# Kernel tuning notes

Measured on AMD Instinct MI355X. Metric: run time of the kernel, lower is better.

The kernel has to match this reference:

```python
import jax, jax.numpy as jnp
import numpy as np

D = 1024
N_HEAD = 16
D_HEAD = D // N_HEAD
EPS = 1e-6


def setup_inputs() -> dict:
    key = jax.random.key(0)
    k1, k2, k3 = jax.random.split(key, 3)
    x = jax.random.normal(k1, (4, 1024, D), dtype=jnp.float32)
    # Linear weights stored as (in, out); y = x @ W
    Wqkv = jax.random.normal(k2, (D, 3 * D), dtype=jnp.float32) * (1.0 / np.sqrt(D))
    Wo = jax.random.normal(k3, (D, D), dtype=jnp.float32) * (1.0 / np.sqrt(D))
    scale_q = jnp.ones((D_HEAD,), dtype=jnp.float32)
    scale_k = jnp.ones((D_HEAD,), dtype=jnp.float32)
    return {"x": x, "Wqkv": Wqkv, "Wo": Wo, "scale_q": scale_q, "scale_k": scale_k}


def _rmsnorm_global(x, scale):
    # NOTE: faithful to source: mean over ALL elements (scalar RMS), not per-vector.
    rms = jnp.sqrt(jnp.mean(x * x))
    return (x / (rms + EPS)) * scale  # scale broadcasts over last dim (d_head)


def reference(x, Wqkv, Wo, scale_q, scale_k):
    b, s, d = x.shape
    qkv = x @ Wqkv  # (b, s, 3d)
    q, k, v = jnp.split(qkv, 3, axis=-1)
    q = q.reshape(b, s, N_HEAD, D_HEAD)
    k = k.reshape(b, s, N_HEAD, D_HEAD)
    v = v.reshape(b, s, N_HEAD, D_HEAD)
    q = _rmsnorm_global(q, scale_q)
    k = _rmsnorm_global(k, scale_k)
    # NOTE: no 1/sqrt(d_head) scaling, no mask (faithful to source)
    attn = jnp.einsum('bqhd,bkhd->bhqk', q, k)
    attn = jax.nn.softmax(attn, axis=-1)
    z = jnp.einsum('bhqk,bkhd->bqhd', attn, v)
    z = z.reshape(b, s, d)
    return z @ Wo
```

## Files before the change

kernel.cpp:

```cpp
#include <hip/hip_runtime.h>

typedef float f32x4 __attribute__((ext_vector_type(4)));
typedef short bf16x8 __attribute__((ext_vector_type(8)));
typedef _Float16 f16x8 __attribute__((ext_vector_type(8)));
typedef unsigned short u16;

__device__ __forceinline__ u16 f2bf(float f) {
  unsigned int u = __float_as_uint(f);
  u = u + 0x7fffu + ((u >> 16) & 1u);
  return (u16)(u >> 16);
}
__device__ __forceinline__ float bf2f(u16 h) {
  return __uint_as_float(((unsigned int)h) << 16);
}
__device__ __forceinline__ u16 f2h(float f) {
  _Float16 h = (_Float16)f;
  union { _Float16 h; u16 u; } cv;
  cv.h = h;
  return cv.u;
}

typedef unsigned int as1_uint __attribute__((address_space(1)));
typedef unsigned int as3_uint __attribute__((address_space(3)));
__device__ __forceinline__ void gl_lds16(const void* g, void* l) {
  __builtin_amdgcn_global_load_lds((as1_uint*)g, (as3_uint*)l, 16, 0, 0);
}


__global__ __launch_bounds__(256) void conv_x_kernel(const float* __restrict__ x,
                                                     u16* __restrict__ Xp) {
  const int g = blockIdx.x * 256 + threadIdx.x;
  const int o = g * 8;
  const int slab = o >> 17;
  const int rem = o & 131071;
  const int kstep = rem >> 12;
  const int rem2 = rem & 4095;
  const int r = rem2 >> 5;
  const int cp = (rem2 & 31) >> 3;
  const int c = cp ^ ((r >> 1) & 3);
  const int s = slab * 128 + r;
  const int k = kstep * 32 + c * 8;
  const float4 v0 = *(const float4*)&x[(size_t)s * 1024 + k];
  const float4 v1 = *(const float4*)&x[(size_t)s * 1024 + k + 4];
  ushort4 a, b;
  a.x = f2h(v0.x); a.y = f2h(v0.y); a.z = f2h(v0.z); a.w = f2h(v0.w);
  b.x = f2h(v1.x); b.y = f2h(v1.y); b.z = f2h(v1.z); b.w = f2h(v1.w);
  *(ushort4*)&Xp[o] = a;
  *(ushort4*)&Xp[o + 4] = b;
}

__global__ __launch_bounds__(256) void conv_w_kernel(
    const float* __restrict__ src, int ncols, u16* __restrict__ dst) {
  __shared__ float tl[64][132];
  const int t = threadIdx.x;
  const int slab = blockIdx.x, kg = blockIdx.y;
  const int n0 = slab * 128, k0 = kg * 64;
#pragma unroll
  for (int i = 0; i < 8; i++) {
    const int fidx = i * 256 + t;
    const int r = fidx >> 5, c4 = (fidx & 31) * 4;
    *(float4*)&tl[r][c4] = *(const float4*)&src[(size_t)(k0 + r) * ncols + n0 + c4];
  }
  __syncthreads();
  const size_t base = (size_t)slab * 131072 + (size_t)(kg * 2) * 4096;
#pragma unroll
  for (int i = 0; i < 4; i++) {
    const int g = i * 256 + t;
    const int img = g >> 9, ci = g & 511;
    const int r = ci >> 2, cp = ci & 3;
    const int c = cp ^ ((r >> 1) & 3);
    const int klc = img * 32 + c * 8;
    ushort4 h0, h1;
    float v[8];
#pragma unroll
    for (int e = 0; e < 8; e++) v[e] = tl[klc + e][r];
    h0.x = f2h(v[0]); h0.y = f2h(v[1]); h0.z = f2h(v[2]); h0.w = f2h(v[3]);
    h1.x = f2h(v[4]); h1.y = f2h(v[5]); h1.z = f2h(v[6]); h1.w = f2h(v[7]);
    *(ushort4*)&dst[base + g * 8] = h0;
    *(ushort4*)&dst[base + g * 8 + 4] = h1;
  }
}

__global__ __launch_bounds__(256) void gemm_qkv_kernel(
    const u16* __restrict__ Xp, const u16* __restrict__ Wp,
    u16* __restrict__ qf, u16* __restrict__ kf, u16* __restrict__ vT,
    const float* __restrict__ scale_q, const float* __restrict__ scale_k,
    float* __restrict__ sums) {
  __shared__ u16 Xs0[4096], Ws0[4096], Xs1[4096], Ws1[4096];
  const int tid = threadIdx.x, wv = tid >> 6, lane = tid & 63;
  const int lm = lane & 15, quad = lane >> 4;
  const int L = blockIdx.x;
  const int xcd = L & 7, idx = L >> 3;
  const int rr = idx & 7, cc8 = idx >> 3;
  const int bmS = (xcd & 3) * 8 + rr;
  const int bnS = (xcd >> 2) * 12 + cc8;
  const bool is_v = (bnS >= 16);
  const int wr = (wv >> 1) * 64, wc = (wv & 1) * 64;
  const int fq = (quad ^ ((lm >> 1) & 3)) * 8;
  const u16* Xg = Xp + (size_t)bmS * 131072;
  const u16* Wg = Wp + (size_t)bnS * 131072;
  const int dof0 = (wv * 2) * 512, dof1 = (wv * 2 + 1) * 512;
  const f32x4 z4 = {0.f, 0.f, 0.f, 0.f};
  f32x4 acc[4][4];
#pragma unroll
  for (int i = 0; i < 4; i++)
#pragma unroll
    for (int j = 0; j < 4; j++) acc[i][j] = z4;

#define ISSUE(t, Xs, Ws)                                   \
  do {                                                     \
    const size_t tb_ = (size_t)(t) * 4096;                 \
    gl_lds16(Xg + tb_ + dof0 + lane * 8, &Xs[dof0]);       \
    gl_lds16(Xg + tb_ + dof1 + lane * 8, &Xs[dof1]);       \
    gl_lds16(Wg + tb_ + dof0 + lane * 8, &Ws[dof0]);       \
    gl_lds16(Wg + tb_ + dof1 + lane * 8, &Ws[dof1]);       \
  } while (0)

  const u16* A0 = is_v ? Xs0 : Ws0;
  const u16* B0 = is_v ? Ws0 : Xs0;
  const u16* A1 = is_v ? Xs1 : Ws1;
  const u16* B1 = is_v ? Ws1 : Xs1;

  ISSUE(0, Xs0, Ws0);
  for (int t = 0; t < 32; t += 2) {
    __syncthreads();
    {
      f16x8 afr[4], bfr[4];
#pragma unroll
      for (int mi = 0; mi < 4; mi++)
        afr[mi] = *(const f16x8*)&A0[(wr + mi * 16 + lm) * 32 + fq];
#pragma unroll
      for (int ni = 0; ni < 4; ni++)
        bfr[ni] = *(const f16x8*)&B0[(wc + ni * 16 + lm) * 32 + fq];
      ISSUE(t + 1, Xs1, Ws1);
#pragma unroll
      for (int mi = 0; mi < 4; mi++)
#pragma unroll
        for (int ni = 0; ni < 4; ni++)
          acc[mi][ni] = __builtin_amdgcn_mfma_f32_16x16x32_f16(
              afr[mi], bfr[ni], acc[mi][ni], 0, 0, 0);
    }
    __syncthreads();
    {
      f16x8 afr[4], bfr[4];
#pragma unroll
      for (int mi = 0; mi < 4; mi++)
        afr[mi] = *(const f16x8*)&A1[(wr + mi * 16 + lm) * 32 + fq];
#pragma unroll
      for (int ni = 0; ni < 4; ni++)
        bfr[ni] = *(const f16x8*)&B1[(wc + ni * 16 + lm) * 32 + fq];
      if (t + 2 < 32) ISSUE(t + 2, Xs0, Ws0);
#pragma unroll
      for (int mi = 0; mi < 4; mi++)
#pragma unroll
        for (int ni = 0; ni < 4; ni++)
          acc[mi][ni] = __builtin_amdgcn_mfma_f32_16x16x32_f16(
              afr[mi], bfr[ni], acc[mi][ni], 0, 0, 0);
    }
  }
#undef ISSUE

  const int bn = bnS * 128, bm = bmS * 128;
  if (!is_v) {
    const bool is_k = (bnS >= 8);
    u16* dst = is_k ? kf : qf;
    float ss = 0.f;
#pragma unroll
    for (int mi = 0; mi < 4; mi++) {
      const int col0 = bn + wr + mi * 16 + quad * 4;
      const int hh = (col0 >> 6) & 15, d0 = col0 & 63;
      const int dhi = d0 >> 5, cc = (d0 & 31) >> 3, eo = d0 & 7;
      float sc[4] = {1.f, 1.f, 1.f, 1.f};
      if (is_k) {
        const float4 sq = *(const float4*)&scale_q[d0];
        const float4 sk = *(const float4*)&scale_k[d0];
        sc[0] = sq.x * sk.x; sc[1] = sq.y * sk.y;
        sc[2] = sq.z * sk.z; sc[3] = sq.w * sk.w;
      }
#pragma unroll
      for (int ni = 0; ni < 4; ni++) {
        const int s = bm + wc + ni * 16 + lm;
        const int b = s >> 10, sl = s & 1023, st = sl >> 6, r = sl & 63;
        const size_t off = ((size_t)((b * 16 + hh) * 16 + st)) * 4096 +
                           dhi * 2048 + r * 32 + ((cc ^ ((r >> 1) & 3)) * 8) + eo;
        ushort4 h4;
#pragma unroll
        for (int i = 0; i < 4; i++) {
          const float a = acc[mi][ni][i];
          ss += a * a;
          const u16 hv = f2h(a * sc[i]);
          if (i == 0) h4.x = hv;
          else if (i == 1) h4.y = hv;
          else if (i == 2) h4.z = hv;
          else h4.w = hv;
        }
        *(ushort4*)&dst[off] = h4;
      }
    }
#pragma unroll
    for (int m = 32; m >= 1; m >>= 1) ss += __shfl_xor(ss, m, 64);
    if (lane == 0) atomicAdd(&sums[is_k ? 1 : 0], ss);
  } else {
#pragma unroll
    for (int ni = 0; ni < 4; ni++) {
      const int col = (bn - 2048) + wc + ni * 16 + lm;
      const int d = col & 63, hh = col >> 6;
#pragma unroll
      for (int mi = 0; mi < 4; mi++) {
        const int s0 = bm + wr + mi * 16 + quad * 4;
        const int b = s0 >> 10, sl = s0 & 1023, st = sl >> 6;
        const int sh = (sl & 63) >> 5, cc = (sl & 31) >> 3, eo = sl & 7;
        const size_t off = ((size_t)((b * 16 + hh) * 16 + st)) * 4096 +
                           sh * 2048 + d * 32 + ((cc ^ ((d >> 1) & 3)) * 8) + eo;
        ushort4 v4;
        v4.x = f2bf(acc[mi][ni][0]);
        v4.y = f2bf(acc[mi][ni][1]);
        v4.z = f2bf(acc[mi][ni][2]);
        v4.w = f2bf(acc[mi][ni][3]);
        *(ushort4*)&vT[off] = v4;
      }
    }
  }
}

__global__ __launch_bounds__(256) void attn_kernel(
    const u16* __restrict__ qf, const u16* __restrict__ kf,
    const u16* __restrict__ vT, const float* __restrict__ sums,
    u16* __restrict__ z) {
  __shared__ u16 Ks0[4096], Vs0[4096], Ks1[4096], Vs1[4096];
  __shared__ u16 pb[4][2][16][64];
  const int tid = threadIdx.x, wv = tid >> 6, lane = tid & 63;
  const int lm = lane & 15, quad = lane >> 4;
  const int fq = (quad ^ ((lm >> 1) & 3)) * 8;
  const int L = blockIdx.x;
  const int xcd = L & 7, idx = L >> 3;
  const int qt8 = idx & 7, p = idx >> 3;
  const int pair = xcd * 8 + p;
  const int hh = pair & 15, b = pair >> 4;
  const float inv_rq = 1.f / (sqrtf(sums[0] * (1.f / 4194304.f)) + 1e-6f);
  const float inv_rk = 1.f / (sqrtf(sums[1] * (1.f / 4194304.f)) + 1e-6f);
  const float cs = inv_rq * inv_rk;
  const size_t hb = ((size_t)(b * 16 + hh)) * 65536;
  const u16* Kg = kf + hb;
  const u16* Vg = vT + hb;
  const int dof = wv * 1024;

  f16x8 aF[2][2];
#pragma unroll
  for (int qs = 0; qs < 2; qs++) {
    const int soff = wv * 32 + qs * 16;
    const size_t qb = hb + (size_t)(qt8 * 2 + (soff >> 6)) * 4096 +
                      (size_t)((soff & 63) + lm) * 32 + fq;
    aF[qs][0] = *(const f16x8*)&qf[qb];
    aF[qs][1] = *(const f16x8*)&qf[qb + 2048];
  }
  const f32x4 zz = {0.f, 0.f, 0.f, 0.f};
  f32x4 zac[2][4];
#pragma unroll
  for (int qs = 0; qs < 2; qs++)
#pragma unroll
    for (int dt = 0; dt < 4; dt++) zac[qs][dt] = zz;
  float rs[2] = {0.f, 0.f};

#define AISSUE(it, Ks, Vs)                                    \
  do {                                                        \
    const size_t tb_ = (size_t)(it) * 4096;                   \
    gl_lds16(Kg + tb_ + dof + lane * 8, &Ks[dof]);            \
    gl_lds16(Kg + tb_ + dof + 512 + lane * 8, &Ks[dof + 512]);\
    gl_lds16(Vg + tb_ + dof + lane * 8, &Vs[dof]);            \
    gl_lds16(Vg + tb_ + dof + 512 + lane * 8, &Vs[dof + 512]);\
  } while (0)

#define ATTN_BODY(it, Ks, Vs, Kn, Vn, do_issue)                               \
  do {                                                                        \
                                         \
    f16x8 kf0[4], kf1[4];                                                     \
    bf16x8 bv[2][4];                                                          \
_Pragma("unroll")                                                             \
    for (int nt = 0; nt < 4; nt++) {                                          \
      const int ro = (nt * 16 + lm) * 32 + fq;                                \
      kf0[nt] = *(const f16x8*)&Ks[ro];                                       \
      kf1[nt] = *(const f16x8*)&Ks[2048 + ro];                                \
    }                                                                         \
_Pragma("unroll")                                                             \
    for (int ch = 0; ch < 2; ch++)                                            \
_Pragma("unroll")                                                             \
      for (int dt = 0; dt < 4; dt++)                                          \
        bv[ch][dt] = *(const bf16x8*)&Vs[ch * 2048 + (dt * 16 + lm) * 32 + fq];\
    if (do_issue) AISSUE((it) + 1, Kn, Vn);                                   \
               \
_Pragma("unroll")                                                             \
    for (int qs = 0; qs < 2; qs++) {                                          \
_Pragma("unroll")                                                             \
      for (int nt = 0; nt < 4; nt++) {                                        \
        f32x4 c = zz;                                                         \
        c = __builtin_amdgcn_mfma_f32_16x16x32_f16(kf0[nt], aF[qs][0], c, 0, 0, 0);\
        c = __builtin_amdgcn_mfma_f32_16x16x32_f16(kf1[nt], aF[qs][1], c, 0, 0, 0);\
        const int k4 = nt * 4 + quad;                                         \
        const int sw = (k4 & 8) | ((k4 ^ lm) & 7);                            \
        ushort4 pw;                                                           \
        float p0 = __expf(c[0] * cs - 60.f);                                  \
        float p1 = __expf(c[1] * cs - 60.f);                                  \
        float p2 = __expf(c[2] * cs - 60.f);                                  \
        float p3 = __expf(c[3] * cs - 60.f);                                  \
        rs[qs] += (p0 + p1) + (p2 + p3);                                      \
        pw.x = f2bf(p0); pw.y = f2bf(p1); pw.z = f2bf(p2); pw.w = f2bf(p3);   \
        *(ushort4*)&pb[wv][qs][lm][sw * 4] = pw;                              \
      }                                                                       \
    }                                                                         \
           \
_Pragma("unroll")                                                             \
    for (int ch = 0; ch < 2; ch++) {                                          \
_Pragma("unroll")                                                             \
      for (int qs = 0; qs < 2; qs++) {                                        \
        const int k4a = ch * 8 + quad * 2, k4b = k4a + 1;                     \
        const ushort4 lo4 =                                                   \
            *(const ushort4*)&pb[wv][qs][lm][((k4a & 8) | ((k4a ^ lm) & 7)) * 4];\
        const ushort4 hi4 =                                                   \
            *(const ushort4*)&pb[wv][qs][lm][((k4b & 8) | ((k4b ^ lm) & 7)) * 4];\
        bf16x8 ap;                                                            \
        ap[0] = (short)lo4.x; ap[1] = (short)lo4.y;                           \
        ap[2] = (short)lo4.z; ap[3] = (short)lo4.w;                           \
        ap[4] = (short)hi4.x; ap[5] = (short)hi4.y;                           \
        ap[6] = (short)hi4.z; ap[7] = (short)hi4.w;                           \
_Pragma("unroll")                                                             \
        for (int dt = 0; dt < 4; dt++)                                        \
          zac[qs][dt] = __builtin_amdgcn_mfma_f32_16x16x32_bf16(              \
              bv[ch][dt], ap, zac[qs][dt], 0, 0, 0);                          \
      }                                                                       \
    }                                                                         \
  } while (0)

  AISSUE(0, Ks0, Vs0);
  for (int it = 0; it < 16; it += 2) {
    __syncthreads();
    ATTN_BODY(it, Ks0, Vs0, Ks1, Vs1, true);
    __syncthreads();
    ATTN_BODY(it + 1, Ks1, Vs1, Ks0, Vs0, (it + 2 < 16));
  }
#undef AISSUE
#undef ATTN_BODY

#pragma unroll
  for (int qs = 0; qs < 2; qs++) {
    rs[qs] += __shfl_xor(rs[qs], 16, 64);
    rs[qs] += __shfl_xor(rs[qs], 32, 64);
  }
  const int slab = b * 8 + qt8;
#pragma unroll
  for (int qs = 0; qs < 2; qs++) {
    const float inv = 1.f / rs[qs];
    const int r = wv * 32 + qs * 16 + lm;
#pragma unroll
    for (int dt = 0; dt < 4; dt++) {
      const int kstep = hh * 2 + (dt >> 1);
      const int d0 = dt * 16 + quad * 4;
      const int cc = (d0 & 31) >> 3, eo = d0 & 7;
      const size_t off = ((size_t)(slab * 32 + kstep)) * 4096 + r * 32 +
                         ((cc ^ ((r >> 1) & 3)) * 8) + eo;
      ushort4 o;
      o.x = f2h(zac[qs][dt][0] * inv);
      o.y = f2h(zac[qs][dt][1] * inv);
      o.z = f2h(zac[qs][dt][2] * inv);
      o.w = f2h(zac[qs][dt][3] * inv);
      *(ushort4*)&z[off] = o;
    }
  }
}

__global__ __launch_bounds__(256) void gemm_o_kernel(const u16* __restrict__ Wop,
                                                     const u16* __restrict__ zp,
                                                     float* __restrict__ out) {
  __shared__ u16 As0[4096], Bs0[4096], As1[4096], Bs1[4096];
  const int tid = threadIdx.x, wv = tid >> 6, lane = tid & 63;
  const int lm = lane & 15, quad = lane >> 4;
  const int wr = (wv >> 1) * 64, wc = (wv & 1) * 64;
  const int fq = (quad ^ ((lm >> 1) & 3)) * 8;
  const int L = blockIdx.x;
  const int xcd = L & 7, idx = L >> 3;
  const int rr = idx & 7, cc8 = idx >> 3;
  const int zpS = (xcd & 3) * 8 + rr;
  const int woS = (xcd >> 2) * 4 + cc8;
  const u16* Ag = Wop + (size_t)woS * 131072;
  const u16* Bg = zp + (size_t)zpS * 131072;
  const int dof0 = (wv * 2) * 512, dof1 = (wv * 2 + 1) * 512;
  const f32x4 z4 = {0.f, 0.f, 0.f, 0.f};
  f32x4 acc[4][4];
#pragma unroll
  for (int i = 0; i < 4; i++)
#pragma unroll
    for (int j = 0; j < 4; j++) acc[i][j] = z4;

#define ISSUE(t, As, Bs)                                   \
  do {                                                     \
    const size_t tb_ = (size_t)(t) * 4096;                 \
    gl_lds16(Ag + tb_ + dof0 + lane * 8, &As[dof0]);       \
    gl_lds16(Ag + tb_ + dof1 + lane * 8, &As[dof1]);       \
    gl_lds16(Bg + tb_ + dof0 + lane * 8, &Bs[dof0]);       \
    gl_lds16(Bg + tb_ + dof1 + lane * 8, &Bs[dof1]);       \
  } while (0)
#define GBODY(As, Bs)                                                     \
  do {                                                                    \
    f16x8 afr[4], bfr[4];                                                 \
_Pragma("unroll")                                                         \
    for (int mi = 0; mi < 4; mi++)                                        \
      afr[mi] = *(const f16x8*)&As[(wr + mi * 16 + lm) * 32 + fq];        \
_Pragma("unroll")                                                         \
    for (int ni = 0; ni < 4; ni++)                                        \
      bfr[ni] = *(const f16x8*)&Bs[(wc + ni * 16 + lm) * 32 + fq];        \
    DO_ISSUE;                                                             \
_Pragma("unroll")                                                         \
    for (int mi = 0; mi < 4; mi++)                                        \
_Pragma("unroll")                                                         \
      for (int ni = 0; ni < 4; ni++)                                      \
        acc[mi][ni] = __builtin_amdgcn_mfma_f32_16x16x32_f16(             \
            afr[mi], bfr[ni], acc[mi][ni], 0, 0, 0);                      \
  } while (0)

  ISSUE(0, As0, Bs0);
  for (int t = 0; t < 32; t += 2) {
    __syncthreads();
#define DO_ISSUE ISSUE(t + 1, As1, Bs1)
    GBODY(As0, Bs0);
#undef DO_ISSUE
    __syncthreads();
#define DO_ISSUE if (t + 2 < 32) ISSUE(t + 2, As0, Bs0)
    GBODY(As1, Bs1);
#undef DO_ISSUE
  }
#undef ISSUE
#undef GBODY

#pragma unroll
  for (int mi = 0; mi < 4; mi++) {
    const int col0 = woS * 128 + wr + mi * 16 + quad * 4;
#pragma unroll
    for (int ni = 0; ni < 4; ni++) {
      const int s = zpS * 128 + wc + ni * 16 + lm;
      const float4 o = {acc[mi][ni][0], acc[mi][ni][1], acc[mi][ni][2],
                        acc[mi][ni][3]};
      *(float4*)&out[(size_t)s * 1024 + col0] = o;
    }
  }
}

extern "C" void kernel_launch(void* const* d_in, const int* in_sizes, int n_in,
                              void* d_out, int out_size, void* d_ws,
                              size_t ws_size, hipStream_t stream) {
  (void)in_sizes; (void)n_in; (void)out_size; (void)ws_size;
  const float* x = (const float*)d_in[0];
  const float* Wqkv = (const float*)d_in[1];
  const float* Wo = (const float*)d_in[2];
  const float* scale_q = (const float*)d_in[3];
  const float* scale_k = (const float*)d_in[4];
  float* out = (float*)d_out;

  char* ws = (char*)d_ws;
  u16* qf = (u16*)(ws + 0);
  u16* kf = (u16*)(ws + 8388608);
  u16* Xp = (u16*)(ws + 16777216);
  u16* vT = (u16*)(ws + 25165824);
  u16* Wp = (u16*)(ws + 33554432);
  u16* zp = Xp;
  u16* Wop = Wp;
  float* sums = (float*)(ws + 39845888);

  conv_x_kernel<<<2048, 256, 0, stream>>>(x, Xp);
  conv_w_kernel<<<dim3(24, 16), 256, 0, stream>>>(Wqkv, 3072, Wp);
  hipMemsetAsync(sums, 0, 2 * sizeof(float), stream);
  gemm_qkv_kernel<<<768, 256, 0, stream>>>(Xp, Wp, qf, kf, vT,
                                           scale_q, scale_k, sums);
  conv_w_kernel<<<dim3(8, 16), 256, 0, stream>>>(Wo, 1024, Wop);
  attn_kernel<<<512, 256, 0, stream>>>(qf, kf, vT, sums, zp);
  gemm_o_kernel<<<256, 256, 0, stream>>>(Wop, zp, out);
}
```

Baseline: 197.7 us.

## Enlarge QKV GEMM tiles to 256x256 with 8 waves and explicit phase pipeline

The QKV projection GEMM moves from 128x128 tiles with 4 waves to 256x256 tiles with 8 waves (192 blocks). Each K-tile is split into four sub-phases with manual vmcnt/lgkmcnt waits, raw s_barrier, sched_barrier and setprio around the MFMA bursts. Global-to-LDS staging of the next tile is interleaved between phases. The aim is more operand reuse per LDS byte and better overlap of loads with MFMA, at the cost of fewer blocks (192 on a 256-CU device), more LDS (128KB) and higher register pressure.

```diff
diff --git a/kernel.cpp b/kernel.cpp
--- a/kernel.cpp
+++ b/kernel.cpp
@@ -81,93 +81,134 @@
   }
 }
 
-__global__ __launch_bounds__(256) void gemm_qkv_kernel(
+__global__ __launch_bounds__(512, 2) void gemm_qkv_kernel(
     const u16* __restrict__ Xp, const u16* __restrict__ Wp,
     u16* __restrict__ qf, u16* __restrict__ kf, u16* __restrict__ vT,
     const float* __restrict__ scale_q, const float* __restrict__ scale_k,
     float* __restrict__ sums) {
-  __shared__ u16 Xs0[4096], Ws0[4096], Xs1[4096], Ws1[4096];
+  __shared__ u16 SA[2][4][4096];
+  __shared__ u16 SB[2][4][4096];
   const int tid = threadIdx.x, wv = tid >> 6, lane = tid & 63;
   const int lm = lane & 15, quad = lane >> 4;
+  const int wvM = wv >> 2, wvN = wv & 3;
   const int L = blockIdx.x;
   const int xcd = L & 7, idx = L >> 3;
-  const int rr = idx & 7, cc8 = idx >> 3;
-  const int bmS = (xcd & 3) * 8 + rr;
-  const int bnS = (xcd >> 2) * 12 + cc8;
-  const bool is_v = (bnS >= 16);
-  const int wr = (wv >> 1) * 64, wc = (wv & 1) * 64;
+  const int bmT = (xcd & 3) * 4 + (idx & 3);
+  const int bnT = (xcd >> 2) * 6 + (idx >> 2);
+  const bool is_v = (bnT >= 8);
   const int fq = (quad ^ ((lm >> 1) & 3)) * 8;
-  const u16* Xg = Xp + (size_t)bmS * 131072;
-  const u16* Wg = Wp + (size_t)bnS * 131072;
-  const int dof0 = (wv * 2) * 512, dof1 = (wv * 2 + 1) * 512;
+  const int aOff = lm * 32 + fq;
+  const u16* Xg = Xp + (size_t)bmT * 262144;
+  const u16* Wg = Wp + (size_t)bnT * 262144;
+  int bSub[4];
+#pragma unroll
+  for (int n = 0; n < 4; n++) {
+    const int wn = wvN * 64 + n * 16;
+    bSub[n] = ((wn >> 7) * 4096) + (wn & 127) * 32;
+  }
+  const u16* Ard = is_v ? &SA[0][0][0] : &SB[0][0][0];
+  const u16* Brd = is_v ? &SB[0][0][0] : &SA[0][0][0];
+
   const f32x4 z4 = {0.f, 0.f, 0.f, 0.f};
-  f32x4 acc[4][4];
-#pragma unroll
-  for (int i = 0; i < 4; i++)
+  f32x4 acc[8][4];
+#pragma unroll
+  for (int i = 0; i < 8; i++)
 #pragma unroll
     for (int j = 0; j < 4; j++) acc[i][j] = z4;
 
-#define ISSUE(t, Xs, Ws)                                   \
-  do {                                                     \
-    const size_t tb_ = (size_t)(t) * 4096;                 \
-    gl_lds16(Xg + tb_ + dof0 + lane * 8, &Xs[dof0]);       \
-    gl_lds16(Xg + tb_ + dof1 + lane * 8, &Xs[dof1]);       \
-    gl_lds16(Wg + tb_ + dof0 + lane * 8, &Ws[dof0]);       \
-    gl_lds16(Wg + tb_ + dof1 + lane * 8, &Ws[dof1]);       \
+#define VMCNT4() asm volatile("s_waitcnt vmcnt(4)" ::: "memory")
+#define VMCNT0() asm volatile("s_waitcnt vmcnt(0)" ::: "memory")
+#define LGKM0() asm volatile("s_waitcnt lgkmcnt(0)" ::: "memory")
+#define CFENCE() asm volatile("" ::: "memory")
+
+#define QSTAGE(tt, nb, k2, sl)                                               \
+  do {                                                                       \
+    const size_t go_ = (size_t)(sl)*131072 + (size_t)(2 * (tt) + (k2)) * 4096\
+                       + wv * 512 + lane * 8;                                \
+    gl_lds16(Xg + go_, &SA[nb][(k2)*2 + (sl)][wv * 512]);                    \
+    gl_lds16(Wg + go_, &SB[nb][(k2)*2 + (sl)][wv * 512]);                    \
   } while (0)
 
-  const u16* A0 = is_v ? Xs0 : Ws0;
-  const u16* B0 = is_v ? Ws0 : Xs0;
-  const u16* A1 = is_v ? Xs1 : Ws1;
-  const u16* B1 = is_v ? Ws1 : Xs1;
-
-  ISSUE(0, Xs0, Ws0);
-  for (int t = 0; t < 32; t += 2) {
-    __syncthreads();
-    {
-      f16x8 afr[4], bfr[4];
-#pragma unroll
-      for (int mi = 0; mi < 4; mi++)
-        afr[mi] = *(const f16x8*)&A0[(wr + mi * 16 + lm) * 32 + fq];
-#pragma unroll
-      for (int ni = 0; ni < 4; ni++)
-        bfr[ni] = *(const f16x8*)&B0[(wc + ni * 16 + lm) * 32 + fq];
-      ISSUE(t + 1, Xs1, Ws1);
-#pragma unroll
-      for (int mi = 0; mi < 4; mi++)
-#pragma unroll
-        for (int ni = 0; ni < 4; ni++)
-          acc[mi][ni] = __builtin_amdgcn_mfma_f32_16x16x32_f16(
-              afr[mi], bfr[ni], acc[mi][ni], 0, 0, 0);
-    }
-    __syncthreads();
-    {
-      f16x8 afr[4], bfr[4];
-#pragma unroll
-      for (int mi = 0; mi < 4; mi++)
-        afr[mi] = *(const f16x8*)&A1[(wr + mi * 16 + lm) * 32 + fq];
-#pragma unroll
-      for (int ni = 0; ni < 4; ni++)
-        bfr[ni] = *(const f16x8*)&B1[(wc + ni * 16 + lm) * 32 + fq];
-      if (t + 2 < 32) ISSUE(t + 2, Xs0, Ws0);
-#pragma unroll
-      for (int mi = 0; mi < 4; mi++)
-#pragma unroll
-        for (int ni = 0; ni < 4; ni++)
-          acc[mi][ni] = __builtin_amdgcn_mfma_f32_16x16x32_f16(
-              afr[mi], bfr[ni], acc[mi][ni], 0, 0, 0);
-    }
-  }
-#undef ISSUE
-
-  const int bn = bnS * 128, bm = bmS * 128;
+#define READ_A(BUF, k2, mq)                                                  \
+  _Pragma("unroll")                                                          \
+  for (int i = 0; i < 4; i++)                                                \
+    afr[i] = *(const f16x8*)&Ard[(BUF)*16384 + ((k2)*2 + wvM) * 4096 +       \
+                                 ((mq)*4 + i) * 512 + aOff];
+#define READ_B(BUF, k2)                                                      \
+  _Pragma("unroll")                                                          \
+  for (int n = 0; n < 4; n++)                                                \
+    bfr[n] = *(const f16x8*)&Brd[(BUF)*16384 + (k2)*8192 + bSub[n] + aOff];
+#define MFMA16(mq)                                                           \
+  _Pragma("unroll")                                                          \
+  for (int i = 0; i < 4; i++)                                                \
+    _Pragma("unroll")                                                        \
+    for (int n = 0; n < 4; n++)                                              \
+      acc[(mq)*4 + i][n] = __builtin_amdgcn_mfma_f32_16x16x32_f16(           \
+          afr[i], bfr[n], acc[(mq)*4 + i][n], 0, 0, 0);
+
+#define PH_TOP(BUF, k2, mq)                                                  \
+  __builtin_amdgcn_s_barrier();                                              \
+  CFENCE();                                                                  \
+  READ_A(BUF, k2, mq)
+#define PH_BOT(mq)                                                           \
+  LGKM0();                                                                   \
+  __builtin_amdgcn_sched_barrier(0);                                         \
+  __builtin_amdgcn_s_setprio(1);                                             \
+  MFMA16(mq);                                                                \
+  __builtin_amdgcn_s_setprio(0)
+
+#define KTILE(BUF, NBUF, t, DOSTAGE, W2)                                     \
+  do {                                                                       \
+    f16x8 afr[4], bfr[4];                                                    \
+                                                   \
+    VMCNT4();                                                                \
+    PH_TOP(BUF, 0, 0);                                                       \
+    READ_B(BUF, 0);                                                          \
+    if (DOSTAGE) QSTAGE((t) + 1, NBUF, 0, 0);                                \
+    PH_BOT(0);                                                               \
+                                                  \
+    PH_TOP(BUF, 0, 1);                                                       \
+    if (DOSTAGE) QSTAGE((t) + 1, NBUF, 0, 1);                                \
+    PH_BOT(1);                                                               \
+                                                   \
+    W2;                                                                      \
+    PH_TOP(BUF, 1, 0);                                                       \
+    READ_B(BUF, 1);                                                          \
+    if (DOSTAGE) QSTAGE((t) + 1, NBUF, 1, 0);                                \
+    PH_BOT(0);                                                               \
+                                                  \
+    PH_TOP(BUF, 1, 1);                                                       \
+    if (DOSTAGE) QSTAGE((t) + 1, NBUF, 1, 1);                                \
+    PH_BOT(1);                                                               \
+  } while (0)
+
+  QSTAGE(0, 0, 0, 0);
+  QSTAGE(0, 0, 0, 1);
+  QSTAGE(0, 0, 1, 0);
+  QSTAGE(0, 0, 1, 1);
+#pragma unroll 1
+  for (int t = 0; t < 14; t += 2) {
+    KTILE(0, 1, t, true, VMCNT4());
+    KTILE(1, 0, t + 1, true, VMCNT4());
+  }
+  KTILE(0, 1, 14, true, VMCNT4());
+  KTILE(1, 0, 15, false, VMCNT0());
+#undef KTILE
+#undef PH_TOP
+#undef PH_BOT
+#undef READ_A
+#undef READ_B
+#undef MFMA16
+#undef QSTAGE
+
+  const int bn = bnT * 256, bm = bmT * 256;
   if (!is_v) {
-    const bool is_k = (bnS >= 8);
+    const bool is_k = (bnT >= 4);
     u16* dst = is_k ? kf : qf;
     float ss = 0.f;
 #pragma unroll
-    for (int mi = 0; mi < 4; mi++) {
-      const int col0 = bn + wr + mi * 16 + quad * 4;
+    for (int mi = 0; mi < 8; mi++) {
+      const int col0 = bn + wvM * 128 + mi * 16 + quad * 4;
       const int hh = (col0 >> 6) & 15, d0 = col0 & 63;
       const int dhi = d0 >> 5, cc = (d0 & 31) >> 3, eo = d0 & 7;
       float sc[4] = {1.f, 1.f, 1.f, 1.f};
@@ -179,7 +220,7 @@
       }
 #pragma unroll
       for (int ni = 0; ni < 4; ni++) {
-        const int s = bm + wc + ni * 16 + lm;
+        const int s = bm + wvN * 64 + ni * 16 + lm;
         const int b = s >> 10, sl = s & 1023, st = sl >> 6, r = sl & 63;
         const size_t off = ((size_t)((b * 16 + hh) * 16 + st)) * 4096 +
                            dhi * 2048 + r * 32 + ((cc ^ ((r >> 1) & 3)) * 8) + eo;
@@ -203,11 +244,11 @@
   } else {
 #pragma unroll
     for (int ni = 0; ni < 4; ni++) {
-      const int col = (bn - 2048) + wc + ni * 16 + lm;
+      const int col = (bn - 2048) + wvN * 64 + ni * 16 + lm;
       const int d = col & 63, hh = col >> 6;
 #pragma unroll
-      for (int mi = 0; mi < 4; mi++) {
-        const int s0 = bm + wr + mi * 16 + quad * 4;
+      for (int mi = 0; mi < 8; mi++) {
+        const int s0 = bm + wvM * 128 + mi * 16 + quad * 4;
         const int b = s0 >> 10, sl = s0 & 1023, st = sl >> 6;
         const int sh = (sl & 63) >> 5, cc = (sl & 31) >> 3, eo = sl & 7;
         const size_t off = ((size_t)((b * 16 + hh) * 16 + st)) * 4096 +
@@ -221,6 +262,10 @@
       }
     }
   }
+#undef VMCNT4
+#undef VMCNT0
+#undef LGKM0
+#undef CFENCE
 }
 
 __global__ __launch_bounds__(256) void attn_kernel(
@@ -468,7 +513,7 @@
   conv_x_kernel<<<2048, 256, 0, stream>>>(x, Xp);
   conv_w_kernel<<<dim3(24, 16), 256, 0, stream>>>(Wqkv, 3072, Wp);
   hipMemsetAsync(sums, 0, 2 * sizeof(float), stream);
-  gemm_qkv_kernel<<<768, 256, 0, stream>>>(Xp, Wp, qf, kf, vT,
+  gemm_qkv_kernel<<<192, 512, 0, stream>>>(Xp, Wp, qf, kf, vT,
                                            scale_q, scale_k, sums);
   conv_w_kernel<<<dim3(8, 16), 256, 0, stream>>>(Wo, 1024, Wop);
   attn_kernel<<<512, 256, 0, stream>>>(qf, kf, vT, sums, zp);
```

New measurement: 182.4 us. -7.8%, faster.
